# Optimization experiments

Hardware: AMD Instinct MI355X
Metric: run time of the kernel (lower is better)

## Reference

```python
import jax, jax.numpy as jnp
import numpy as np

B, H, S, D = 2, 16, 2048, 64


def setup_inputs() -> dict:
    key = jax.random.key(0)
    kq, kk, kv = jax.random.split(key, 3)
    q = jax.random.normal(kq, (B, H, S, D), dtype=jnp.float32)
    k = jax.random.normal(kk, (B, H, S, D), dtype=jnp.float32)
    v = jax.random.normal(kv, (B, H, S, D), dtype=jnp.float32)
    # causal mask: 1.0 where attention is DISALLOWED (strictly upper triangle)
    mask = jnp.triu(jnp.ones((S, S), dtype=jnp.float32), k=1)[None, None, :, :]
    return {"k": k, "q": q, "v": v, "mask": mask}


def reference(k, q, v, mask):
    d_k = jnp.asarray(k.shape[-1], dtype=jnp.float32)
    # scores: [B, H, S, S]
    scores = jnp.einsum("bhqd,bhkd->bhqk", q, k) / jnp.sqrt(d_k)
    scores = scores + mask * (-1e9)
    weights = jax.nn.softmax(scores, axis=-1)
    # attention output: [B, H, S, D]
    return jnp.einsum("bhqk,bhkd->bhqd", weights, v)
```

## Files before the change

kernel.cpp:

```cpp
#include <hip/hip_runtime.h>
#include <hip/hip_bf16.h>

typedef unsigned short ushort_t;
typedef __attribute__((ext_vector_type(8))) short v8s;
typedef __attribute__((ext_vector_type(4))) float v4f;

#define SEQ   2048
#define DH    64
#define NHEAD 32
#define BK    32
#define NT64  32
#define KSTR  72
#define VSTR  40

#if __has_builtin(__builtin_amdgcn_exp2f)
#define EXP2(x) __builtin_amdgcn_exp2f(x)
#else
#define EXP2(x) exp2f(x)
#endif

__device__ __forceinline__ unsigned pkbf(float lo, float hi) {
    __hip_bfloat162 h = __float22bfloat162_rn(make_float2(lo, hi));
    union { __hip_bfloat162 h; unsigned u; } c; c.h = h; return c.u;
}

__device__ __forceinline__ v8s load8_bf_scaled(const float* p, float sc) {
    float4 a = *(const float4*)p;
    float4 b = *(const float4*)(p + 4);
    union { v8s v; unsigned u[4]; } t;
    t.u[0] = pkbf(a.x * sc, a.y * sc);
    t.u[1] = pkbf(a.z * sc, a.w * sc);
    t.u[2] = pkbf(b.x * sc, b.y * sc);
    t.u[3] = pkbf(b.z * sc, b.w * sc);
    return t.v;
}

__device__ __forceinline__ void process_tile_T(
    int kb, int myq0, int quad, int l15,
    v8s qa0, v8s qa1,
    v8s ka00, v8s ka01, v8s ka10, v8s ka11,
    v8s vb0, v8s vb1, v8s vb2, v8s vb3,
    v4f& a0, v4f& a1, v4f& a2, v4f& a3, float& ls)
{
    const v4f z = {0.f, 0.f, 0.f, 0.f};
    v4f s0 = __builtin_amdgcn_mfma_f32_16x16x32_bf16(ka00, qa0, z, 0, 0, 0);
    s0     = __builtin_amdgcn_mfma_f32_16x16x32_bf16(ka01, qa1, s0, 0, 0, 0);
    v4f s1 = __builtin_amdgcn_mfma_f32_16x16x32_bf16(ka10, qa0, z, 0, 0, 0);
    s1     = __builtin_amdgcn_mfma_f32_16x16x32_bf16(ka11, qa1, s1, 0, 0, 0);

    float p0[4], p1[4];
    if (kb + BK <= myq0) {
        #pragma unroll
        for (int r = 0; r < 4; ++r) { p0[r] = EXP2(s0[r]); p1[r] = EXP2(s1[r]); }
    } else {
        const int qrow = myq0 + l15;
        #pragma unroll
        for (int r = 0; r < 4; ++r) {
            p0[r] = (kb + 4 * quad + r      <= qrow) ? EXP2(s0[r]) : 0.f;
            p1[r] = (kb + 16 + 4 * quad + r <= qrow) ? EXP2(s1[r]) : 0.f;
        }
    }
    #pragma unroll
    for (int r = 0; r < 4; ++r) ls += p0[r] + p1[r];

    union { v8s v; unsigned u[4]; } pa;
    pa.u[0] = pkbf(p0[0], p0[1]); pa.u[1] = pkbf(p0[2], p0[3]);
    pa.u[2] = pkbf(p1[0], p1[1]); pa.u[3] = pkbf(p1[2], p1[3]);
    a0 = __builtin_amdgcn_mfma_f32_16x16x32_bf16(pa.v, vb0, a0, 0, 0, 0);
    a1 = __builtin_amdgcn_mfma_f32_16x16x32_bf16(pa.v, vb1, a1, 0, 0, 0);
    a2 = __builtin_amdgcn_mfma_f32_16x16x32_bf16(pa.v, vb2, a2, 0, 0, 0);
    a3 = __builtin_amdgcn_mfma_f32_16x16x32_bf16(pa.v, vb3, a3, 0, 0, 0);
}

__global__ __launch_bounds__(256, 2)
void attn_causal_kernel(const float* __restrict__ Kg,
                        const float* __restrict__ Qg,
                        const float* __restrict__ Vg,
                        float* __restrict__ Og) {
    __shared__ alignas(16) ushort_t Kt[2][BK * KSTR];
    __shared__ alignas(16) ushort_t Vt[2][DH * VSTR];

    const int i    = blockIdx.x;
    const int head = i & 31;
    const int pair = i >> 5;
    const int qbL  = pair * 64;
    const int qbH  = (NT64 - 1 - pair) * 64;
    const int tid  = threadIdx.x;
    const int w    = tid >> 6;
    const int lane = tid & 63;
    const int l15  = lane & 15;
    const int quad = lane >> 4;

    const int myq0L = qbL + w * 16, qmaxL = myq0L + 15;
    const int myq0H = qbH + w * 16, qmaxH = myq0H + 15;
    const size_t hb = (size_t)head * SEQ * DH;

    const float QSC = 0.125f * 1.4426950408889634f;
    v8s qaL0, qaL1, qaH0, qaH1;
    {
        const float* qpL = Qg + hb + (size_t)(myq0L + l15) * DH + quad * 8;
        const float* qpH = Qg + hb + (size_t)(myq0H + l15) * DH + quad * 8;
        qaL0 = load8_bf_scaled(qpL, QSC);  qaL1 = load8_bf_scaled(qpL + 32, QSC);
        qaH0 = load8_bf_scaled(qpH, QSC);  qaH1 = load8_bf_scaled(qpH + 32, QSC);
    }

    v4f aL0 = {0.f,0.f,0.f,0.f}, aL1 = aL0, aL2 = aL0, aL3 = aL0;
    v4f aH0 = aL0, aH1 = aL0, aH2 = aL0, aH3 = aL0;
    float lsL = 0.f, lsH = 0.f;

    const int ntiles = (qbH + 64) / BK;

    const int sk_kpos = tid >> 3;
    const int sk_d    = (tid & 7) * 8;
    const int sv_d = tid & 63;

    const float* kbase  = Kg + hb + (size_t)sk_kpos * DH + sk_d;
    const float* vbaseA = Vg + hb + (size_t)(4 * w) * DH + sv_d;
    const float* vbaseB = Vg + hb + (size_t)(16 + 4 * w) * DH + sv_d;
    ushort_t* kdst0 = &Kt[0][sk_kpos * KSTR + sk_d];
    ushort_t* vdst0 = &Vt[0][sv_d * VSTR + 8 * w];
    const int KOFS = BK * KSTR;
    const int VOFS = DH * VSTR;

    {
        float4 k0 = *(const float4*)(kbase);
        float4 k1 = *(const float4*)(kbase + 4);
        float va[4], vb[4];
        #pragma unroll
        for (int m = 0; m < 4; ++m) {
            va[m] = vbaseA[(size_t)m * DH];
            vb[m] = vbaseB[(size_t)m * DH];
        }
        union { v8s v; unsigned u[4]; } kc, vc;
        kc.u[0] = pkbf(k0.x, k0.y); kc.u[1] = pkbf(k0.z, k0.w);
        kc.u[2] = pkbf(k1.x, k1.y); kc.u[3] = pkbf(k1.z, k1.w);
        vc.u[0] = pkbf(va[0], va[1]); vc.u[1] = pkbf(va[2], va[3]);
        vc.u[2] = pkbf(vb[0], vb[1]); vc.u[3] = pkbf(vb[2], vb[3]);
        *(v8s*)kdst0 = kc.v;
        *(v8s*)vdst0 = vc.v;
    }
    __syncthreads();

    for (int kt = 0; kt < ntiles; ++kt) {
        const int cur = kt & 1;
        const bool havenext = (kt + 1 < ntiles);

        float4 nk0, nk1; float nva[4], nvb[4];
        if (havenext) {
            const size_t toff = (size_t)(kt + 1) * BK * DH;
            nk0 = *(const float4*)(kbase + toff);
            nk1 = *(const float4*)(kbase + toff + 4);
            #pragma unroll
            for (int m = 0; m < 4; ++m) {
                nva[m] = vbaseA[toff + (size_t)m * DH];
                nvb[m] = vbaseB[toff + (size_t)m * DH];
            }
        }

        const int kb = kt * BK;
        if (kb <= qmaxH) {
            const ushort_t* KB = &Kt[0][cur ? KOFS : 0];
            const ushort_t* VB = &Vt[0][cur ? VOFS : 0];
            union { v8s v; uint4 u; } ka00, ka01, ka10, ka11, vb0, vb1, vb2, vb3;
            ka00.u = *(const uint4*)&KB[(l15)      * KSTR      + quad * 8];
            ka01.u = *(const uint4*)&KB[(l15)      * KSTR + 32 + quad * 8];
            ka10.u = *(const uint4*)&KB[(16 + l15) * KSTR      + quad * 8];
            ka11.u = *(const uint4*)&KB[(16 + l15) * KSTR + 32 + quad * 8];
            vb0.u  = *(const uint4*)&VB[(l15)      * VSTR + quad * 8];
            vb1.u  = *(const uint4*)&VB[(16 + l15) * VSTR + quad * 8];
            vb2.u  = *(const uint4*)&VB[(32 + l15) * VSTR + quad * 8];
            vb3.u  = *(const uint4*)&VB[(48 + l15) * VSTR + quad * 8];

            if (kb <= qmaxL)
                process_tile_T(kb, myq0L, quad, l15, qaL0, qaL1,
                               ka00.v, ka01.v, ka10.v, ka11.v,
                               vb0.v, vb1.v, vb2.v, vb3.v,
                               aL0, aL1, aL2, aL3, lsL);
            process_tile_T(kb, myq0H, quad, l15, qaH0, qaH1,
                           ka00.v, ka01.v, ka10.v, ka11.v,
                           vb0.v, vb1.v, vb2.v, vb3.v,
                           aH0, aH1, aH2, aH3, lsH);
        }

        if (havenext) {
            union { v8s v; unsigned u[4]; } kc, vc;
            kc.u[0] = pkbf(nk0.x, nk0.y); kc.u[1] = pkbf(nk0.z, nk0.w);
            kc.u[2] = pkbf(nk1.x, nk1.y); kc.u[3] = pkbf(nk1.z, nk1.w);
            vc.u[0] = pkbf(nva[0], nva[1]); vc.u[1] = pkbf(nva[2], nva[3]);
            vc.u[2] = pkbf(nvb[0], nvb[1]); vc.u[3] = pkbf(nvb[2], nvb[3]);
            const int nxt = cur ^ 1;
            *(v8s*)(kdst0 + (nxt ? KOFS : 0)) = kc.v;
            *(v8s*)(vdst0 + (nxt ? VOFS : 0)) = vc.v;
        }

        __syncthreads();
    }

    lsL += __shfl_xor(lsL, 16); lsL += __shfl_xor(lsL, 32);
    lsH += __shfl_xor(lsH, 16); lsH += __shfl_xor(lsH, 32);

    #pragma unroll
    for (int r = 0; r < 4; ++r) {
        const float invL = 1.0f / __shfl(lsL, 4 * quad + r);
        const float invH = 1.0f / __shfl(lsH, 4 * quad + r);
        float* opL = Og + hb + (size_t)(myq0L + 4 * quad + r) * DH + l15;
        float* opH = Og + hb + (size_t)(myq0H + 4 * quad + r) * DH + l15;
        opL[0]  = aL0[r] * invL; opL[16] = aL1[r] * invL;
        opL[32] = aL2[r] * invL; opL[48] = aL3[r] * invL;
        opH[0]  = aH0[r] * invH; opH[16] = aH1[r] * invH;
        opH[32] = aH2[r] * invH; opH[48] = aH3[r] * invH;
    }
}

extern "C" void kernel_launch(void* const* d_in, const int* in_sizes, int n_in,
                              void* d_out, int out_size, void* d_ws, size_t ws_size,
                              hipStream_t stream) {
    const float* K = (const float*)d_in[0];
    const float* Q = (const float*)d_in[1];
    const float* V = (const float*)d_in[2];
    float* O = (float*)d_out;
    attn_causal_kernel<<<dim3(512), 256, 0, stream>>>(K, Q, V, O);
}
```

Measured before the change: 144.6 us.

## Use manual bf16 rounding, libm exp2f, and 2D grid over pairs and heads

Replaces the HIP bf16 pack intrinsic with a manual round-to-nearest-even bit trick and swaps the amdgcn exp2 builtin for exp2f. Also changes the launch to a 2D grid (pair, head) instead of a flat grid, which alters block dispatch order: consecutive blocks now share a head rather than a pair. The manual rounding may or may not compile to packed cvt instructions. exp2f may add denormal or range handling over the raw builtin.

After: 170.7 us. +18.1%, slower.

```diff
diff --git a/kernel.cpp b/kernel.cpp
--- a/kernel.cpp
+++ b/kernel.cpp
@@ -13,25 +13,23 @@
 #define KSTR  72
 #define VSTR  40
 
-#if __has_builtin(__builtin_amdgcn_exp2f)
-#define EXP2(x) __builtin_amdgcn_exp2f(x)
-#else
-#define EXP2(x) exp2f(x)
-#endif
-
-__device__ __forceinline__ unsigned pkbf(float lo, float hi) {
-    __hip_bfloat162 h = __float22bfloat162_rn(make_float2(lo, hi));
-    union { __hip_bfloat162 h; unsigned u; } c; c.h = h; return c.u;
+__device__ __forceinline__ ushort_t f2bf(float x) {
+    union { float f; unsigned u; } c; c.f = x;
+    unsigned r = (c.u + 0x7fffu + ((c.u >> 16) & 1u)) >> 16;
+    return (ushort_t)r;
+}
+__device__ __forceinline__ unsigned pk2(float lo, float hi) {
+    return (unsigned)f2bf(lo) | ((unsigned)f2bf(hi) << 16);
 }
 
 __device__ __forceinline__ v8s load8_bf_scaled(const float* p, float sc) {
     float4 a = *(const float4*)p;
     float4 b = *(const float4*)(p + 4);
     union { v8s v; unsigned u[4]; } t;
-    t.u[0] = pkbf(a.x * sc, a.y * sc);
-    t.u[1] = pkbf(a.z * sc, a.w * sc);
-    t.u[2] = pkbf(b.x * sc, b.y * sc);
-    t.u[3] = pkbf(b.z * sc, b.w * sc);
+    t.u[0] = pk2(a.x * sc, a.y * sc);
+    t.u[1] = pk2(a.z * sc, a.w * sc);
+    t.u[2] = pk2(b.x * sc, b.y * sc);
+    t.u[3] = pk2(b.z * sc, b.w * sc);
     return t.v;
 }
 
@@ -51,21 +49,21 @@
     float p0[4], p1[4];
     if (kb + BK <= myq0) {
         #pragma unroll
-        for (int r = 0; r < 4; ++r) { p0[r] = EXP2(s0[r]); p1[r] = EXP2(s1[r]); }
+        for (int r = 0; r < 4; ++r) { p0[r] = exp2f(s0[r]); p1[r] = exp2f(s1[r]); }
     } else {
         const int qrow = myq0 + l15;
         #pragma unroll
         for (int r = 0; r < 4; ++r) {
-            p0[r] = (kb + 4 * quad + r      <= qrow) ? EXP2(s0[r]) : 0.f;
-            p1[r] = (kb + 16 + 4 * quad + r <= qrow) ? EXP2(s1[r]) : 0.f;
+            p0[r] = (kb + 4 * quad + r      <= qrow) ? exp2f(s0[r]) : 0.f;
+            p1[r] = (kb + 16 + 4 * quad + r <= qrow) ? exp2f(s1[r]) : 0.f;
         }
     }
     #pragma unroll
     for (int r = 0; r < 4; ++r) ls += p0[r] + p1[r];
 
     union { v8s v; unsigned u[4]; } pa;
-    pa.u[0] = pkbf(p0[0], p0[1]); pa.u[1] = pkbf(p0[2], p0[3]);
-    pa.u[2] = pkbf(p1[0], p1[1]); pa.u[3] = pkbf(p1[2], p1[3]);
+    pa.u[0] = pk2(p0[0], p0[1]); pa.u[1] = pk2(p0[2], p0[3]);
+    pa.u[2] = pk2(p1[0], p1[1]); pa.u[3] = pk2(p1[2], p1[3]);
     a0 = __builtin_amdgcn_mfma_f32_16x16x32_bf16(pa.v, vb0, a0, 0, 0, 0);
     a1 = __builtin_amdgcn_mfma_f32_16x16x32_bf16(pa.v, vb1, a1, 0, 0, 0);
     a2 = __builtin_amdgcn_mfma_f32_16x16x32_bf16(pa.v, vb2, a2, 0, 0, 0);
@@ -80,9 +78,8 @@
     __shared__ alignas(16) ushort_t Kt[2][BK * KSTR];
     __shared__ alignas(16) ushort_t Vt[2][DH * VSTR];
 
-    const int i    = blockIdx.x;
-    const int head = i & 31;
-    const int pair = i >> 5;
+    const int pair = blockIdx.x;
+    const int head = blockIdx.y;
     const int qbL  = pair * 64;
     const int qbH  = (NT64 - 1 - pair) * 64;
     const int tid  = threadIdx.x;
@@ -132,10 +129,10 @@
             vb[m] = vbaseB[(size_t)m * DH];
         }
         union { v8s v; unsigned u[4]; } kc, vc;
-        kc.u[0] = pkbf(k0.x, k0.y); kc.u[1] = pkbf(k0.z, k0.w);
-        kc.u[2] = pkbf(k1.x, k1.y); kc.u[3] = pkbf(k1.z, k1.w);
-        vc.u[0] = pkbf(va[0], va[1]); vc.u[1] = pkbf(va[2], va[3]);
-        vc.u[2] = pkbf(vb[0], vb[1]); vc.u[3] = pkbf(vb[2], vb[3]);
+        kc.u[0] = pk2(k0.x, k0.y); kc.u[1] = pk2(k0.z, k0.w);
+        kc.u[2] = pk2(k1.x, k1.y); kc.u[3] = pk2(k1.z, k1.w);
+        vc.u[0] = pk2(va[0], va[1]); vc.u[1] = pk2(va[2], va[3]);
+        vc.u[2] = pk2(vb[0], vb[1]); vc.u[3] = pk2(vb[2], vb[3]);
         *(v8s*)kdst0 = kc.v;
         *(v8s*)vdst0 = vc.v;
     }
@@ -184,10 +181,10 @@
 
         if (havenext) {
             union { v8s v; unsigned u[4]; } kc, vc;
-            kc.u[0] = pkbf(nk0.x, nk0.y); kc.u[1] = pkbf(nk0.z, nk0.w);
-            kc.u[2] = pkbf(nk1.x, nk1.y); kc.u[3] = pkbf(nk1.z, nk1.w);
-            vc.u[0] = pkbf(nva[0], nva[1]); vc.u[1] = pkbf(nva[2], nva[3]);
-            vc.u[2] = pkbf(nvb[0], nvb[1]); vc.u[3] = pkbf(nvb[2], nvb[3]);
+            kc.u[0] = pk2(nk0.x, nk0.y); kc.u[1] = pk2(nk0.z, nk0.w);
+            kc.u[2] = pk2(nk1.x, nk1.y); kc.u[3] = pk2(nk1.z, nk1.w);
+            vc.u[0] = pk2(nva[0], nva[1]); vc.u[1] = pk2(nva[2], nva[3]);
+            vc.u[2] = pk2(nvb[0], nvb[1]); vc.u[3] = pk2(nvb[2], nvb[3]);
             const int nxt = cur ^ 1;
             *(v8s*)(kdst0 + (nxt ? KOFS : 0)) = kc.v;
             *(v8s*)(vdst0 + (nxt ? VOFS : 0)) = vc.v;
@@ -219,5 +216,6 @@
     const float* Q = (const float*)d_in[1];
     const float* V = (const float*)d_in[2];
     float* O = (float*)d_out;
-    attn_causal_kernel<<<dim3(512), 256, 0, stream>>>(K, Q, V, O);
-}
+    dim3 grid(NT64 / 2, NHEAD);
+    attn_causal_kernel<<<grid, 256, 0, stream>>>(K, Q, V, O);
+}
```
